# Kernel optimization log

Hardware: AMD Instinct MI355X
Metric: run time of the kernel (lower is better)

Reference implementation:

```python
import jax, jax.numpy as jnp
import numpy as np

N = 50000        # nodes
E = 800000       # directed edges (before self-loops)
F_IN = 128       # input node features
HID = 32         # hidden channels per head
HEADS = 4
NCLS = 8
EPS_BN = 1e-5
NEG_SLOPE = 0.2  # GATConv LeakyReLU default


def setup_inputs() -> dict:
    key = jax.random.key(0)
    ks = jax.random.split(key, 16)
    rn = lambda k, shape, s=0.1: jax.random.normal(k, shape, jnp.float32) * s
    inp = {}
    inp["x"] = jax.random.normal(ks[0], (N, F_IN), jnp.float32)
    inp["edge_index"] = jax.random.randint(ks[1], (2, E), 0, N, dtype=jnp.int32)
    # layer 0: F_IN -> HEADS*HID (concat)
    inp["W0"] = rn(ks[2], (F_IN, HEADS * HID))
    inp["as0"] = rn(ks[3], (HEADS, HID))
    inp["ad0"] = rn(ks[4], (HEADS, HID))
    inp["b0"] = jnp.zeros((HEADS * HID,), jnp.float32)
    inp["g0"] = jnp.ones((HEADS * HID,), jnp.float32)
    inp["bb0"] = jnp.zeros((HEADS * HID,), jnp.float32)
    inp["rm0"] = jnp.zeros((HEADS * HID,), jnp.float32)
    inp["rv0"] = jnp.ones((HEADS * HID,), jnp.float32)
    # layer 1: HEADS*HID -> HEADS*HID (concat)
    inp["W1"] = rn(ks[5], (HEADS * HID, HEADS * HID))
    inp["as1"] = rn(ks[6], (HEADS, HID))
    inp["ad1"] = rn(ks[7], (HEADS, HID))
    inp["b1"] = jnp.zeros((HEADS * HID,), jnp.float32)
    inp["g1"] = jnp.ones((HEADS * HID,), jnp.float32)
    inp["bb1"] = jnp.zeros((HEADS * HID,), jnp.float32)
    inp["rm1"] = jnp.zeros((HEADS * HID,), jnp.float32)
    inp["rv1"] = jnp.ones((HEADS * HID,), jnp.float32)
    # layer 2: HEADS*HID -> NCLS, heads=1, concat=False
    inp["W2"] = rn(ks[8], (HEADS * HID, NCLS))
    inp["as2"] = rn(ks[9], (1, NCLS))
    inp["ad2"] = rn(ks[10], (1, NCLS))
    inp["b2"] = jnp.zeros((NCLS,), jnp.float32)
    return inp


def gat_conv(x, src, dst, W, att_s, att_d, bias, H, C, concat):
    """PyG-style GATConv (eval mode, self-loops already appended to src/dst)."""
    n = x.shape[0]
    h = (x @ W).reshape(n, H, C)                       # [N,H,C]
    a_s = (h * att_s).sum(-1)                          # [N,H]
    a_d = (h * att_d).sum(-1)                          # [N,H]
    e = jax.nn.leaky_relu(a_s[src] + a_d[dst], NEG_SLOPE)  # [E,H]
    # numerically-stable segment softmax over incoming edges of each dst node
    m = jax.ops.segment_max(e, dst, num_segments=n)
    m = jnp.where(jnp.isfinite(m), m, 0.0)
    ex = jnp.exp(e - m[dst])
    den = jax.ops.segment_sum(ex, dst, num_segments=n)
    alpha = ex / (den[dst] + 1e-16)                    # [E,H]
    out = jax.ops.segment_sum(h[src] * alpha[:, :, None], dst, num_segments=n)  # [N,H,C]
    out = out.reshape(n, H * C) if concat else out.mean(axis=1)
    return out + bias


def bn_eval(x, g, b, rm, rv):
    return (x - rm) * jax.lax.rsqrt(rv + EPS_BN) * g + b


def reference(x, edge_index, W0, as0, ad0, b0, g0, bb0, rm0, rv0,
              W1, as1, ad1, b1, g1, bb1, rm1, rv1, W2, as2, ad2, b2):
    n = x.shape[0]
    loop = jnp.arange(n, dtype=edge_index.dtype)       # self-loops (PyG default)
    src = jnp.concatenate([edge_index[0], loop])
    dst = jnp.concatenate([edge_index[1], loop])
    h = gat_conv(x, src, dst, W0, as0, ad0, b0, HEADS, HID, True)
    h = jax.nn.elu(bn_eval(h, g0, bb0, rm0, rv0))
    h = gat_conv(h, src, dst, W1, as1, ad1, b1, HEADS, HID, True)
    h = jax.nn.elu(bn_eval(h, g1, bb1, rm1, rv1))
    h = gat_conv(h, src, dst, W2, as2, ad2, b2, 1, NCLS, False)
    return jax.nn.log_softmax(h, axis=1)
```

## Files before the change

kernel.cpp:

```cpp
#include <hip/hip_runtime.h>
#include <math.h>

#define N_NODES 50000
#define N_EDGES 800000
#define ET (N_EDGES + N_NODES)
#define NEG 0.2f
#define EPS_BN 1e-5f

#define BSH 8
#define NBUCK ((N_NODES + 255) >> BSH)
#define EPB 4096
#define PB ((ET + EPB - 1) / EPB)
#define CAST_B 3125
#define PACK_B 64
#define GB ((N_NODES + 63) / 64)
#define AGG_U 12500
#define G2B ((N_NODES + 255) / 256)
#define PREP_U (PB + CAST_B + 2 * PACK_B)

typedef __attribute__((ext_vector_type(8))) short short8;
typedef __attribute__((ext_vector_type(4))) float f32x4;

__device__ __forceinline__ float lrelu(float e) { return e > 0.f ? e : NEG * e; }
__device__ __forceinline__ float bflo(unsigned u) { return __uint_as_float(u << 16); }
__device__ __forceinline__ float bfhi(unsigned u) { return __uint_as_float(u & 0xffff0000u); }
__device__ __forceinline__ unsigned f2bf(float f) {
    unsigned b = __float_as_uint(f);
    return (b + 0x7fffu + ((b >> 16) & 1u)) >> 16;
}

struct GatParams {
    const int* ei;
    const float* x;
    const float *W0, *as0, *ad0, *b0, *g0, *bb0, *rm0, *rv0;
    const float *W1, *as1, *ad1, *b1, *g1, *bb1, *rm1, *rv1;
    const float *W2, *as2, *ad2, *b2;
    float* out;
    unsigned short *xb, *Hb, *Xb, *W0p, *W1p;
    int *offs, *boffs, *bcur, *ssrc, *hists;
    int2* pairs;
    float *asn, *adn, *h2;
};


__global__ __launch_bounds__(256) void k_prep(GatParams p) {
    __shared__ unsigned h[NBUCK];
    int u = blockIdx.x, tid = threadIdx.x;
    if (u < PB) {
        for (int i = tid; i < NBUCK; i += 256) h[i] = 0;
        __syncthreads();
        int e0 = u * EPB;
        #pragma unroll
        for (int k = 0; k < EPB / 256; k++) {
            int e = e0 + k * 256 + tid;
            if (e < ET) {
                int d = (e < N_EDGES) ? p.ei[N_EDGES + e] : (e - N_EDGES);
                atomicAdd(&h[d >> BSH], 1u);
            }
        }
        __syncthreads();
        for (int i = tid; i < NBUCK; i += 256)
            p.hists[u * NBUCK + i] = (int)h[i];
    } else if (u < PB + CAST_B) {
        int i = (u - PB) * 256 + tid;
        const float4* px = (const float4*)p.x + (size_t)i * 2;
        float4 a = px[0], c = px[1];
        uint4 o;
        o.x = f2bf(a.x) | (f2bf(a.y) << 16);
        o.y = f2bf(a.z) | (f2bf(a.w) << 16);
        o.z = f2bf(c.x) | (f2bf(c.y) << 16);
        o.w = f2bf(c.z) | (f2bf(c.w) << 16);
        ((uint4*)p.xb)[i] = o;
    } else {
        int pb = u - PB - CAST_B;
        const float* W = (pb < PACK_B) ? p.W0 : p.W1;
        unsigned short* Wp = (pb < PACK_B) ? p.W0p : p.W1p;
        int o = (pb & (PACK_B - 1)) * 256 + tid;
        int j = o & 7, lane = (o >> 3) & 63, kc = (o >> 9) & 3, t = o >> 11;
        int k = kc * 32 + ((lane >> 4) << 3) + j;
        int n = t * 16 + (lane & 15);
        Wp[o] = (unsigned short)f2bf(W[k * 128 + n]);
    }
}

__global__ __launch_bounds__(256) void k_scan(GatParams p) {
    __shared__ int s[256];
    int tid = threadIdx.x;
    int v = 0;
    if (tid < NBUCK) {
        const int* hp = p.hists + tid;
        #pragma unroll 8
        for (int uu = 0; uu < PB; uu++) v += hp[uu * NBUCK];
    }
    s[tid] = v;
    __syncthreads();
    for (int off = 1; off < 256; off <<= 1) {
        int x = (tid >= off) ? s[tid - off] : 0;
        __syncthreads();
        s[tid] += x;
        __syncthreads();
    }
    int excl = s[tid] - v;
    if (tid < NBUCK) { p.boffs[tid] = excl; p.bcur[tid] = excl; }
    if (tid == 0) { p.boffs[NBUCK] = ET; p.offs[N_NODES] = ET; }
}

__global__ __launch_bounds__(256) void k_partition(GatParams p) {
    __shared__ unsigned hist[NBUCK];
    __shared__ unsigned base[NBUCK];
    int tid = threadIdx.x;
    int e0 = blockIdx.x * EPB;
    for (int i = tid; i < NBUCK; i += 256) hist[i] = 0;
    __syncthreads();
    #pragma unroll
    for (int k = 0; k < EPB / 256; k++) {
        int e = e0 + k * 256 + tid;
        if (e < ET) {
            int d = (e < N_EDGES) ? p.ei[N_EDGES + e] : (e - N_EDGES);
            atomicAdd(&hist[d >> BSH], 1u);
        }
    }
    __syncthreads();
    for (int i = tid; i < NBUCK; i += 256) {
        unsigned hh = hist[i];
        base[i] = hh ? (unsigned)atomicAdd(&p.bcur[i], (int)hh) : 0u;
        hist[i] = 0;
    }
    __syncthreads();
    #pragma unroll
    for (int k = 0; k < EPB / 256; k++) {
        int e = e0 + k * 256 + tid;
        if (e < ET) {
            int s, d;
            if (e < N_EDGES) { s = p.ei[e]; d = p.ei[N_EDGES + e]; }
            else             { s = d = e - N_EDGES; }
            int b = d >> BSH;
            unsigned lpos = atomicAdd(&hist[b], 1u);
            p.pairs[base[b] + lpos] = make_int2(s, d);
        }
    }
}

__global__ __launch_bounds__(256) void k_group(GatParams p) {
    __shared__ int cnt[256];
    __shared__ int pfx[256];
    int u = blockIdx.x, tid = threadIdx.x;
    int n0 = u << BSH;
    int base = p.boffs[u], end = p.boffs[u + 1];
    cnt[tid] = 0;
    __syncthreads();
    for (int i = base + tid; i < end; i += 256)
        atomicAdd(&cnt[p.pairs[i].y & 255], 1);
    __syncthreads();
    int v = cnt[tid];
    pfx[tid] = v;
    __syncthreads();
    for (int off = 1; off < 256; off <<= 1) {
        int x = (tid >= off) ? pfx[tid - off] : 0;
        __syncthreads();
        pfx[tid] += x;
        __syncthreads();
    }
    int excl = pfx[tid] - v;
    if (n0 + tid < N_NODES) p.offs[n0 + tid] = base + excl;
    cnt[tid] = excl;
    __syncthreads();
    for (int i = base + tid; i < end; i += 256) {
        int2 pr = p.pairs[i];
        int pos = atomicAdd(&cnt[pr.y & 255], 1);
        p.ssrc[base + pos] = pr.x;
    }
}


__global__ __launch_bounds__(256) void k_gemm(GatParams p, int layer) {
    __shared__ float tiles[64 * 132];
    const unsigned short* Ab = (layer == 0) ? p.xb : p.Xb;
    const unsigned short* Wp = (layer == 0) ? p.W0p : p.W1p;
    const float* att_s = (layer == 0) ? p.as0 : p.as1;
    const float* att_d = (layer == 0) ? p.ad0 : p.ad1;
    int tid = threadIdx.x;
    int wv = tid >> 6, lane = tid & 63;
    int base = blockIdx.x * 64;
    int mrow = base + wv * 16 + (lane & 15);
    if (mrow >= N_NODES) mrow = N_NODES - 1;
    int koff = (lane >> 4) * 8;

    f32x4 acc[8];
    #pragma unroll
    for (int t = 0; t < 8; t++) acc[t] = (f32x4){0.f, 0.f, 0.f, 0.f};
    #pragma unroll
    for (int kc = 0; kc < 4; kc++) {
        short8 a = *(const short8*)(Ab + (size_t)mrow * 128 + kc * 32 + koff);
        #pragma unroll
        for (int t = 0; t < 8; t++) {
            short8 b = *(const short8*)(Wp + (((t * 4 + kc) * 64 + lane) << 3));
            acc[t] = __builtin_amdgcn_mfma_f32_16x16x32_bf16(a, b, acc[t], 0, 0, 0);
        }
    }
    int rbase = wv * 16 + (lane >> 4) * 4;
    int col = lane & 15;
    #pragma unroll
    for (int t = 0; t < 8; t++)
        #pragma unroll
        for (int r = 0; r < 4; r++)
            tiles[(rbase + r) * 132 + t * 16 + col] = acc[t][r];
    __syncthreads();

    #pragma unroll
    for (int it = 0; it < 4; it++) {
        int uu = tid + it * 256;
        int rl = uu >> 4, cg4 = uu & 15;
        int row = base + rl;
        if (row < N_NODES) {
            const float* pt = tiles + rl * 132 + cg4 * 8;
            float4 v0 = *(const float4*)(pt);
            float4 v1 = *(const float4*)(pt + 4);
            uint4 o;
            o.x = f2bf(v0.x) | (f2bf(v0.y) << 16);
            o.y = f2bf(v0.z) | (f2bf(v0.w) << 16);
            o.z = f2bf(v1.x) | (f2bf(v1.y) << 16);
            o.w = f2bf(v1.z) | (f2bf(v1.w) << 16);
            *(uint4*)(p.Hb + (size_t)row * 128 + cg4 * 8) = o;
        }
    }
    {
        int rl = tid >> 2, hd = tid & 3;
        int row = base + rl;
        if (row < N_NODES) {
            const float* hrow = tiles + rl * 132 + hd * 32;
            const float* as = att_s + hd * 32;
            const float* ad = att_d + hd * 32;
            float ps = 0.f, pd = 0.f;
            #pragma unroll
            for (int i = 0; i < 8; i++) {
                float4 hv = *(const float4*)(hrow + i * 4);
                float4 sv = *(const float4*)(as + i * 4);
                float4 dv = *(const float4*)(ad + i * 4);
                ps += hv.x * sv.x + hv.y * sv.y + hv.z * sv.z + hv.w * sv.w;
                pd += hv.x * dv.x + hv.y * dv.y + hv.z * dv.z + hv.w * dv.w;
            }
            p.asn[row * 4 + hd] = ps;
            p.adn[row * 4 + hd] = pd;
        }
    }
}


__global__ __launch_bounds__(256) void k_agg(GatParams p, int layer) {
    __shared__ int2 sP[4 * 4 * 72];
    const float* bias  = (layer == 0) ? p.b0  : p.b1;
    const float* gamma = (layer == 0) ? p.g0  : p.g1;
    const float* beta  = (layer == 0) ? p.bb0 : p.bb1;
    const float* rmean = (layer == 0) ? p.rm0 : p.rm1;
    const float* rvar  = (layer == 0) ? p.rv0 : p.rv1;
    int tid = threadIdx.x;
    int wv = tid >> 6, lane = tid & 63;
    int half = lane >> 5, cl = lane & 31, hsel = cl >> 3;
    const char* hbase = (const char*)p.Hb + cl * 8;
    int2* st0 = sP + (wv * 4 + 0) * 72;
    int2* st1 = sP + (wv * 4 + 1) * 72;
    int2* st2 = sP + (wv * 4 + 2) * 72;
    int2* st3 = sP + (wv * 4 + 3) * 72;
    const int2* pp = sP + (wv * 4 + hsel) * 72;

    int node = blockIdx.x * 4 + wv;
    int beg = p.offs[node], deg = p.offs[node + 1] - beg;
    float4 ad4 = *(const float4*)(p.adn + node * 4);
    float a0 = 0.f, a1 = 0.f, a2 = 0.f, a3 = 0.f, denl = 0.f;

    for (int base0 = 0; base0 < deg; base0 += 64) {
        int j = base0 + lane;
        int soff = 0;
        float4 w4v = make_float4(0.f, 0.f, 0.f, 0.f);
        if (j < deg) {
            int s = p.ssrc[beg + j];
            soff = s << 8;
            float4 a = *(const float4*)(p.asn + s * 4);
            w4v.x = __expf(lrelu(a.x + ad4.x));
            w4v.y = __expf(lrelu(a.y + ad4.y));
            w4v.z = __expf(lrelu(a.z + ad4.z));
            w4v.w = __expf(lrelu(a.w + ad4.w));
        }
        st0[lane] = make_int2(soff, __float_as_int(w4v.x));
        st1[lane] = make_int2(soff, __float_as_int(w4v.y));
        st2[lane] = make_int2(soff, __float_as_int(w4v.z));
        st3[lane] = make_int2(soff, __float_as_int(w4v.w));
        int cnt = deg - base0; if (cnt > 64) cnt = 64;

        int i = 0;
        for (; i + 16 <= cnt; i += 16) {
            int2 p0 = pp[i + 0 + half],  p1 = pp[i + 2 + half];
            int2 p2 = pp[i + 4 + half],  p3 = pp[i + 6 + half];
            int2 p4 = pp[i + 8 + half],  p5 = pp[i + 10 + half];
            int2 p6 = pp[i + 12 + half], p7 = pp[i + 14 + half];
            uint2 u0 = *(const uint2*)(hbase + (unsigned)p0.x);
            uint2 u1 = *(const uint2*)(hbase + (unsigned)p1.x);
            uint2 u2 = *(const uint2*)(hbase + (unsigned)p2.x);
            uint2 u3 = *(const uint2*)(hbase + (unsigned)p3.x);
            uint2 u4 = *(const uint2*)(hbase + (unsigned)p4.x);
            uint2 u5 = *(const uint2*)(hbase + (unsigned)p5.x);
            uint2 u6 = *(const uint2*)(hbase + (unsigned)p6.x);
            uint2 u7 = *(const uint2*)(hbase + (unsigned)p7.x);
            float w0 = __int_as_float(p0.y), w1 = __int_as_float(p1.y);
            float w2 = __int_as_float(p2.y), w3 = __int_as_float(p3.y);
            float w4 = __int_as_float(p4.y), w5 = __int_as_float(p5.y);
            float w6 = __int_as_float(p6.y), w7 = __int_as_float(p7.y);
            denl += w0 + w1 + w2 + w3 + w4 + w5 + w6 + w7;
            a0 += w0 * bflo(u0.x); a1 += w0 * bfhi(u0.x); a2 += w0 * bflo(u0.y); a3 += w0 * bfhi(u0.y);
            a0 += w1 * bflo(u1.x); a1 += w1 * bfhi(u1.x); a2 += w1 * bflo(u1.y); a3 += w1 * bfhi(u1.y);
            a0 += w2 * bflo(u2.x); a1 += w2 * bfhi(u2.x); a2 += w2 * bflo(u2.y); a3 += w2 * bfhi(u2.y);
            a0 += w3 * bflo(u3.x); a1 += w3 * bfhi(u3.x); a2 += w3 * bflo(u3.y); a3 += w3 * bfhi(u3.y);
            a0 += w4 * bflo(u4.x); a1 += w4 * bfhi(u4.x); a2 += w4 * bflo(u4.y); a3 += w4 * bfhi(u4.y);
            a0 += w5 * bflo(u5.x); a1 += w5 * bfhi(u5.x); a2 += w5 * bflo(u5.y); a3 += w5 * bfhi(u5.y);
            a0 += w6 * bflo(u6.x); a1 += w6 * bfhi(u6.x); a2 += w6 * bflo(u6.y); a3 += w6 * bfhi(u6.y);
            a0 += w7 * bflo(u7.x); a1 += w7 * bfhi(u7.x); a2 += w7 * bflo(u7.y); a3 += w7 * bfhi(u7.y);
        }
        for (; i < cnt; i += 4) {
            int2 p0 = pp[i + half], p1 = pp[i + 2 + half];
            uint2 u0 = *(const uint2*)(hbase + (unsigned)p0.x);
            uint2 u1 = *(const uint2*)(hbase + (unsigned)p1.x);
            float w0 = __int_as_float(p0.y), w1 = __int_as_float(p1.y);
            denl += w0 + w1;
            a0 += w0 * bflo(u0.x); a1 += w0 * bfhi(u0.x); a2 += w0 * bflo(u0.y); a3 += w0 * bfhi(u0.y);
            a0 += w1 * bflo(u1.x); a1 += w1 * bfhi(u1.x); a2 += w1 * bflo(u1.y); a3 += w1 * bfhi(u1.y);
        }
    }
    a0 += __shfl_xor(a0, 32); a1 += __shfl_xor(a1, 32);
    a2 += __shfl_xor(a2, 32); a3 += __shfl_xor(a3, 32);
    denl += __shfl_xor(denl, 32);
    if (half == 0) {
        float inv = 1.f / (denl + 1e-16f);
        int c0 = cl * 4;
        float4 bi = *(const float4*)(bias + c0);
        float4 gm = *(const float4*)(gamma + c0);
        float4 bt = *(const float4*)(beta + c0);
        float4 rm = *(const float4*)(rmean + c0);
        float4 rv = *(const float4*)(rvar + c0);
        float o0 = a0 * inv + bi.x, o1 = a1 * inv + bi.y;
        float o2 = a2 * inv + bi.z, o3 = a3 * inv + bi.w;
        o0 = (o0 - rm.x) * rsqrtf(rv.x + EPS_BN) * gm.x + bt.x;
        o1 = (o1 - rm.y) * rsqrtf(rv.y + EPS_BN) * gm.y + bt.y;
        o2 = (o2 - rm.z) * rsqrtf(rv.z + EPS_BN) * gm.z + bt.z;
        o3 = (o3 - rm.w) * rsqrtf(rv.w + EPS_BN) * gm.w + bt.w;
        o0 = (o0 > 0.f) ? o0 : expm1f(o0);
        o1 = (o1 > 0.f) ? o1 : expm1f(o1);
        o2 = (o2 > 0.f) ? o2 : expm1f(o2);
        o3 = (o3 > 0.f) ? o3 : expm1f(o3);
        uint2 ob;
        ob.x = f2bf(o0) | (f2bf(o1) << 16);
        ob.y = f2bf(o2) | (f2bf(o3) << 16);
        *(uint2*)(p.Xb + (size_t)node * 128 + c0) = ob;
    }
}


__global__ __launch_bounds__(256) void k_gemm2(GatParams p) {
    __shared__ float sW[128 * 8];
    __shared__ float sas[8], sad[8];
    int tid = threadIdx.x;
    for (int i = tid; i < 1024; i += 256) sW[i] = p.W2[i];
    if (tid < 8) { sas[tid] = p.as2[tid]; sad[tid] = p.ad2[tid]; }
    __syncthreads();
    int node = blockIdx.x * 256 + tid;
    if (node >= N_NODES) return;
    const uint4* xr = (const uint4*)(p.Xb + (size_t)node * 128);
    float acc[8];
    #pragma unroll
    for (int c = 0; c < 8; c++) acc[c] = 0.f;
    for (int k8 = 0; k8 < 16; k8++) {
        uint4 uu = xr[k8];
        float f[8] = { bflo(uu.x), bfhi(uu.x), bflo(uu.y), bfhi(uu.y),
                       bflo(uu.z), bfhi(uu.z), bflo(uu.w), bfhi(uu.w) };
        int kb = k8 * 8;
        #pragma unroll
        for (int q = 0; q < 8; q++)
            #pragma unroll
            for (int c = 0; c < 8; c++)
                acc[c] += f[q] * sW[(kb + q) * 8 + c];
    }
    float ps = 0.f, pd = 0.f;
    #pragma unroll
    for (int c = 0; c < 8; c++) {
        p.h2[(size_t)node * 8 + c] = acc[c];
        ps += acc[c] * sas[c];
        pd += acc[c] * sad[c];
    }
    p.asn[node] = ps;
    p.adn[node] = pd;
}


__global__ __launch_bounds__(256) void k_agg2(GatParams p) {
    __shared__ int2 sP[4 * 64];
    int tid = threadIdx.x;
    int wv = tid >> 6, lane = tid & 63;
    int g = lane >> 3, c = lane & 7;
    int node = blockIdx.x * 4 + wv;
    int beg = p.offs[node], end = p.offs[node + 1];
    int deg = end - beg;
    float adv = p.adn[node];
    float den = 0.f, acc = 0.f;
    int2* ws = sP + wv * 64;
    for (int base = 0; base < deg; base += 64) {
        int j = base + lane;
        int s = 0; float w = 0.f;
        if (j < deg) {
            s = p.ssrc[beg + j];
            w = __expf(lrelu(p.asn[s] + adv));
            den += w;
        }
        ws[lane] = make_int2(s, __float_as_int(w));
        int cnt = deg - base; if (cnt > 64) cnt = 64;
        int i = 0;
        for (; i + 16 <= cnt; i += 16) {
            int2 p0 = ws[i + g];
            int2 p1 = ws[i + 8 + g];
            acc += __int_as_float(p0.y) * p.h2[(((unsigned)p0.x) << 3) + c];
            acc += __int_as_float(p1.y) * p.h2[(((unsigned)p1.x) << 3) + c];
        }
        for (; i < cnt; i += 8) {
            int2 p0 = ws[i + g];
            acc += __int_as_float(p0.y) * p.h2[(((unsigned)p0.x) << 3) + c];
        }
    }
    acc += __shfl_xor(acc, 8); acc += __shfl_xor(acc, 16); acc += __shfl_xor(acc, 32);
    #pragma unroll
    for (int off = 32; off; off >>= 1) den += __shfl_xor(den, off);
    float o = acc / (den + 1e-16f) + p.b2[c];
    float mx = o;
    mx = fmaxf(mx, __shfl_xor(mx, 1));
    mx = fmaxf(mx, __shfl_xor(mx, 2));
    mx = fmaxf(mx, __shfl_xor(mx, 4));
    float ex = __expf(o - mx);
    float sm = ex;
    sm += __shfl_xor(sm, 1); sm += __shfl_xor(sm, 2); sm += __shfl_xor(sm, 4);
    if (g == 0) p.out[(size_t)node * 8 + c] = o - mx - logf(sm);
}


extern "C" void kernel_launch(void* const* d_in, const int* in_sizes, int n_in,
                              void* d_out, int out_size, void* d_ws, size_t ws_size,
                              hipStream_t stream) {
    GatParams prm;
    prm.ei  = (const int*)d_in[1];
    prm.x   = (const float*)d_in[0];
    prm.W0  = (const float*)d_in[2];
    prm.as0 = (const float*)d_in[3];  prm.ad0 = (const float*)d_in[4];
    prm.b0  = (const float*)d_in[5];  prm.g0  = (const float*)d_in[6];
    prm.bb0 = (const float*)d_in[7];  prm.rm0 = (const float*)d_in[8];
    prm.rv0 = (const float*)d_in[9];
    prm.W1  = (const float*)d_in[10];
    prm.as1 = (const float*)d_in[11]; prm.ad1 = (const float*)d_in[12];
    prm.b1  = (const float*)d_in[13]; prm.g1  = (const float*)d_in[14];
    prm.bb1 = (const float*)d_in[15]; prm.rm1 = (const float*)d_in[16];
    prm.rv1 = (const float*)d_in[17];
    prm.W2  = (const float*)d_in[18];
    prm.as2 = (const float*)d_in[19]; prm.ad2 = (const float*)d_in[20];
    prm.b2  = (const float*)d_in[21];
    prm.out = (float*)d_out;

    char* w = (char*)d_ws;
    size_t off = 0;
    auto carve = [&](size_t bytes) {
        void* p = w + off;
        off += (bytes + 255) & ~(size_t)255;
        return p;
    };
    prm.xb    = (unsigned short*)carve((size_t)N_NODES * 128 * 2);
    prm.Hb    = (unsigned short*)carve((size_t)N_NODES * 128 * 2);
    prm.Xb    = (unsigned short*)carve((size_t)N_NODES * 128 * 2);
    prm.W0p   = (unsigned short*)carve(16384 * 2);
    prm.W1p   = (unsigned short*)carve(16384 * 2);
    prm.offs  = (int*)carve((size_t)(N_NODES + 1) * 4);
    prm.boffs = (int*)carve((size_t)(NBUCK + 1) * 4);
    prm.bcur  = (int*)carve((size_t)NBUCK * 4);
    prm.ssrc  = (int*)carve((size_t)ET * 4);
    prm.hists = (int*)carve((size_t)PB * NBUCK * 4);
    prm.pairs = (int2*)carve((size_t)ET * 8);
    prm.asn   = (float*)carve((size_t)N_NODES * 4 * 4);
    prm.adn   = (float*)carve((size_t)N_NODES * 4 * 4);
    prm.h2    = (float*)carve((size_t)N_NODES * 8 * 4);
    (void)ws_size; (void)in_sizes; (void)n_in; (void)out_size;

    k_prep<<<PREP_U, 256, 0, stream>>>(prm);
    k_scan<<<1, 256, 0, stream>>>(prm);
    k_partition<<<PB, 256, 0, stream>>>(prm);
    k_group<<<NBUCK, 256, 0, stream>>>(prm);
    k_gemm<<<GB, 256, 0, stream>>>(prm, 0);
    k_agg<<<AGG_U, 256, 0, stream>>>(prm, 0);
    k_gemm<<<GB, 256, 0, stream>>>(prm, 1);
    k_agg<<<AGG_U, 256, 0, stream>>>(prm, 1);
    k_gemm2<<<G2B, 256, 0, stream>>>(prm);
    k_agg2<<<AGG_U, 256, 0, stream>>>(prm);
}
```

Before: 291.5 us.

## Fold bucket scan into partition and group kernels, drop global atomics

Removes the single-block scan kernel. Each partition block now reads the per-block bucket histograms written by prep, computes the global exclusive scan plus its own prefix, and scatters into deterministic positions without a second histogram pass or global atomics. The group kernel likewise recomputes its bucket base and end from the histograms instead of reading stored offsets. This saves one launch, one histogram pass and the global atomic traffic, at the cost of redundant reads of the histogram table (PB x NBUCK) in every block.

Measured after the change: 290.0 us. No clear change (-0.5%).

```diff
diff --git a/kernel.cpp b/kernel.cpp
--- a/kernel.cpp
+++ b/kernel.cpp
@@ -37,7 +37,7 @@
     const float *W2, *as2, *ad2, *b2;
     float* out;
     unsigned short *xb, *Hb, *Xb, *W0p, *W1p;
-    int *offs, *boffs, *bcur, *ssrc, *hists;
+    int *offs, *ssrc, *hists;
     int2* pairs;
     float *asn, *adn, *h2;
 };
@@ -83,16 +83,22 @@
     }
 }
 
-__global__ __launch_bounds__(256) void k_scan(GatParams p) {
+
+__global__ __launch_bounds__(256) void k_partition(GatParams p) {
     __shared__ int s[256];
-    int tid = threadIdx.x;
-    int v = 0;
+    __shared__ int lcur[NBUCK];
+    int u = blockIdx.x, tid = threadIdx.x;
+
+    int tot = 0, pre = 0;
     if (tid < NBUCK) {
         const int* hp = p.hists + tid;
-        #pragma unroll 8
-        for (int uu = 0; uu < PB; uu++) v += hp[uu * NBUCK];
-    }
-    s[tid] = v;
+        for (int v = 0; v < PB; v++) {
+            int hh = hp[v * NBUCK];
+            tot += hh;
+            if (v < u) pre += hh;
+        }
+    }
+    s[tid] = tot;
     __syncthreads();
     for (int off = 1; off < 256; off <<= 1) {
         int x = (tid >= off) ? s[tid - off] : 0;
@@ -100,53 +106,49 @@
         s[tid] += x;
         __syncthreads();
     }
-    int excl = s[tid] - v;
-    if (tid < NBUCK) { p.boffs[tid] = excl; p.bcur[tid] = excl; }
-    if (tid == 0) { p.boffs[NBUCK] = ET; p.offs[N_NODES] = ET; }
-}
-
-__global__ __launch_bounds__(256) void k_partition(GatParams p) {
-    __shared__ unsigned hist[NBUCK];
-    __shared__ unsigned base[NBUCK];
-    int tid = threadIdx.x;
-    int e0 = blockIdx.x * EPB;
-    for (int i = tid; i < NBUCK; i += 256) hist[i] = 0;
-    __syncthreads();
+    if (tid < NBUCK) lcur[tid] = (s[tid] - tot) + pre;
+    __syncthreads();
+
+    int e0 = u * EPB;
     #pragma unroll
     for (int k = 0; k < EPB / 256; k++) {
         int e = e0 + k * 256 + tid;
         if (e < ET) {
-            int d = (e < N_EDGES) ? p.ei[N_EDGES + e] : (e - N_EDGES);
-            atomicAdd(&hist[d >> BSH], 1u);
-        }
-    }
-    __syncthreads();
-    for (int i = tid; i < NBUCK; i += 256) {
-        unsigned hh = hist[i];
-        base[i] = hh ? (unsigned)atomicAdd(&p.bcur[i], (int)hh) : 0u;
-        hist[i] = 0;
-    }
-    __syncthreads();
-    #pragma unroll
-    for (int k = 0; k < EPB / 256; k++) {
-        int e = e0 + k * 256 + tid;
-        if (e < ET) {
-            int s, d;
-            if (e < N_EDGES) { s = p.ei[e]; d = p.ei[N_EDGES + e]; }
-            else             { s = d = e - N_EDGES; }
-            int b = d >> BSH;
-            unsigned lpos = atomicAdd(&hist[b], 1u);
-            p.pairs[base[b] + lpos] = make_int2(s, d);
-        }
-    }
-}
+            int sv, d;
+            if (e < N_EDGES) { sv = p.ei[e]; d = p.ei[N_EDGES + e]; }
+            else             { sv = d = e - N_EDGES; }
+            int pos = atomicAdd(&lcur[d >> BSH], 1);
+            p.pairs[pos] = make_int2(sv, d);
+        }
+    }
+}
+
 
 __global__ __launch_bounds__(256) void k_group(GatParams p) {
+    __shared__ int s[256];
     __shared__ int cnt[256];
     __shared__ int pfx[256];
+    __shared__ int sBase[2];
     int u = blockIdx.x, tid = threadIdx.x;
+
+    int tot = 0;
+    if (tid < NBUCK) {
+        const int* hp = p.hists + tid;
+        for (int v = 0; v < PB; v++) tot += hp[v * NBUCK];
+    }
+    s[tid] = tot;
+    __syncthreads();
+    for (int off = 1; off < 256; off <<= 1) {
+        int x = (tid >= off) ? s[tid - off] : 0;
+        __syncthreads();
+        s[tid] += x;
+        __syncthreads();
+    }
+    if (tid == u) { sBase[0] = s[tid] - tot; sBase[1] = s[tid]; }
+    __syncthreads();
+    int base = sBase[0], end = sBase[1];
+
     int n0 = u << BSH;
-    int base = p.boffs[u], end = p.boffs[u + 1];
     cnt[tid] = 0;
     __syncthreads();
     for (int i = base + tid; i < end; i += 256)
@@ -163,6 +165,7 @@
     }
     int excl = pfx[tid] - v;
     if (n0 + tid < N_NODES) p.offs[n0 + tid] = base + excl;
+    if (u == 0 && tid == 0) p.offs[N_NODES] = ET;
     cnt[tid] = excl;
     __syncthreads();
     for (int i = base + tid; i < end; i += 256) {
@@ -473,8 +476,6 @@
     prm.W0p   = (unsigned short*)carve(16384 * 2);
     prm.W1p   = (unsigned short*)carve(16384 * 2);
     prm.offs  = (int*)carve((size_t)(N_NODES + 1) * 4);
-    prm.boffs = (int*)carve((size_t)(NBUCK + 1) * 4);
-    prm.bcur  = (int*)carve((size_t)NBUCK * 4);
     prm.ssrc  = (int*)carve((size_t)ET * 4);
     prm.hists = (int*)carve((size_t)PB * NBUCK * 4);
     prm.pairs = (int2*)carve((size_t)ET * 8);
@@ -484,7 +485,6 @@
     (void)ws_size; (void)in_sizes; (void)n_in; (void)out_size;
 
     k_prep<<<PREP_U, 256, 0, stream>>>(prm);
-    k_scan<<<1, 256, 0, stream>>>(prm);
     k_partition<<<PB, 256, 0, stream>>>(prm);
     k_group<<<NBUCK, 256, 0, stream>>>(prm);
     k_gemm<<<GB, 256, 0, stream>>>(prm, 0);
```
